# Kernel tuning notes

Hardware: AMD Instinct MI355X
Metric: run time of the kernel (lower is better)

## Reference

```python
import jax, jax.numpy as jnp
import numpy as np

U_NUM, I_NUM, EMBED, NUM_LAYERS = 100000, 50000, 64, 3
N_NODES = U_NUM + I_NUM
BATCH = 8192


def _build_laplacian(rng):
    # Faithful to buildLaplacianMat: symmetric bipartite rating matrix with
    # D^-1/2 A D^-1/2 normalization (degree = count of nonzeros per row).
    nnz = 2_000_000
    u = rng.integers(0, U_NUM, nnz)
    i = rng.integers(0, I_NUM, nnz)
    lin = np.unique(u.astype(np.int64) * I_NUM + i)  # dedupe (user,item) pairs
    u = (lin // I_NUM).astype(np.int32)
    i = (lin % I_NUM).astype(np.int32)
    rating = rng.integers(1, 6, u.shape[0]).astype(np.float32)
    rows = np.concatenate([u, i + U_NUM])
    cols = np.concatenate([i + U_NUM, u])
    vals = np.concatenate([rating, rating])
    deg = np.bincount(rows, minlength=N_NODES)
    dinv = np.where(deg > 0, deg.astype(np.float64) ** -0.5, 0.0).astype(np.float32)
    vals = dinv[rows] * vals * dinv[cols]
    return rows, cols, vals


def setup_inputs() -> dict:
    key = jax.random.key(0)
    k1, k2 = jax.random.split(key)
    rng = np.random.default_rng(0)
    rows, cols, vals = _build_laplacian(rng)
    # xavier_uniform over [num, embed]: bound = sqrt(6/(fan_in+fan_out))
    bu = float(np.sqrt(6.0 / (U_NUM + EMBED)))
    bi = float(np.sqrt(6.0 / (I_NUM + EMBED)))
    uEmbd = jax.random.uniform(k1, (U_NUM, EMBED), jnp.float32, -bu, bu)
    iEmbd = jax.random.uniform(k2, (I_NUM, EMBED), jnp.float32, -bi, bi)
    userIdx = jnp.asarray(rng.integers(0, U_NUM, BATCH), dtype=jnp.int64)
    itemIdx = jnp.asarray(rng.integers(0, I_NUM, BATCH), dtype=jnp.int64)
    return {
        "uEmbd": uEmbd,
        "iEmbd": iEmbd,
        "lap_rows": jnp.asarray(rows, jnp.int32),
        "lap_cols": jnp.asarray(cols, jnp.int32),
        "lap_vals": jnp.asarray(vals, jnp.float32),
        "userIdx": userIdx,
        "itemIdx": itemIdx,
    }


def _spmm(rows, cols, vals, x):
    # sparse [N,N] @ dense [N,D] via edge-list gather + segment-sum
    return jax.ops.segment_sum(vals[:, None] * x[cols], rows, num_segments=N_NODES)


def reference(uEmbd, iEmbd, lap_rows, lap_cols, lap_vals, userIdx, itemIdx):
    feats = jnp.concatenate([uEmbd, iEmbd], axis=0)  # [N, D]
    acc = feats
    f = feats
    for _ in range(NUM_LAYERS):
        f = _spmm(lap_rows, lap_cols, lap_vals, f)
        acc = acc + f
    final = acc / (NUM_LAYERS + 1)  # mean over stacked layer embeddings
    ue = final[userIdx]                      # [B, D]
    ie = final[itemIdx + U_NUM]              # [B, D]
    return jnp.sum(ue * ie, axis=1)          # [B]
```

## Files before the change

kernel.cpp:

```cpp
#include <hip/hip_runtime.h>

#define U_NUMC 100000
#define I_NUMC 50000
#define NNODES 150000
#define EMB 64
#define NBATCH 8192
#define NB_I ((I_NUMC + 255) / 256)

__global__ __launch_bounds__(256) void k_zero(int* __restrict__ p, int n) {
    int i = blockIdx.x * blockDim.x + threadIdx.x;
    if (i < n) p[i] = 0;
}

__global__ __launch_bounds__(256) void k_uptr(const int* __restrict__ rows1, int E1,
                                              int* __restrict__ uptr) {
    int r = blockIdx.x * blockDim.x + threadIdx.x;
    if (r > U_NUMC) return;
    int lo = 0, hi = E1;
    while (lo < hi) {
        int mid = (lo + hi) >> 1;
        if (rows1[mid] < r) lo = mid + 1; else hi = mid;
    }
    uptr[r] = lo;
}

__global__ __launch_bounds__(256) void k_hist(const int* __restrict__ cols1, int E1,
                                              int* __restrict__ hist) {
    int e = blockIdx.x * blockDim.x + threadIdx.x;
    if (e >= E1) return;
    atomicAdd(&hist[cols1[e] - U_NUMC], 1);
}

__global__ __launch_bounds__(256) void k_scan1(const int* __restrict__ hist,
                                               int* __restrict__ bsum) {
    int b = blockIdx.x, t = threadIdx.x;
    int idx = b * 256 + t;
    int v = (idx < I_NUMC) ? hist[idx] : 0;
    #pragma unroll
    for (int o = 32; o; o >>= 1) v += __shfl_xor(v, o);
    __shared__ int ws4[4];
    if ((t & 63) == 0) ws4[t >> 6] = v;
    __syncthreads();
    if (t == 0) bsum[b] = ws4[0] + ws4[1] + ws4[2] + ws4[3];
}

__global__ __launch_bounds__(256) void k_scan2(const int* __restrict__ bsum,
                                               int* __restrict__ boff,
                                               int* __restrict__ iptr) {
    __shared__ int lds[256];
    int t = threadIdx.x;
    int v = (t < NB_I) ? bsum[t] : 0;
    int x = v;
    #pragma unroll
    for (int o = 1; o < 256; o <<= 1) {
        lds[t] = x; __syncthreads();
        int y = (t >= o) ? lds[t - o] : 0; __syncthreads();
        x += y;
    }
    if (t < NB_I) boff[t] = x - v;
    if (t == 255) iptr[I_NUMC] = x;
}

__global__ __launch_bounds__(256) void k_scan3(const int* __restrict__ hist,
                                               const int* __restrict__ boff,
                                               int* __restrict__ iptr,
                                               int* __restrict__ cursor) {
    __shared__ int lds[256];
    int b = blockIdx.x, t = threadIdx.x;
    int idx = b * 256 + t;
    int v = (idx < I_NUMC) ? hist[idx] : 0;
    int x = v;
    #pragma unroll
    for (int o = 1; o < 256; o <<= 1) {
        lds[t] = x; __syncthreads();
        int y = (t >= o) ? lds[t - o] : 0; __syncthreads();
        x += y;
    }
    if (idx < I_NUMC) {
        int excl = boff[b] + x - v;
        iptr[idx] = excl;
        cursor[idx] = excl;
    }
}

__global__ __launch_bounds__(256) void k_scatter(const int* __restrict__ rows1,
                                                 const int* __restrict__ cols1,
                                                 const float* __restrict__ vals1,
                                                 int E1,
                                                 int* __restrict__ cursor,
                                                 int2* __restrict__ item_uv) {
    const int cls  = blockIdx.x & 7;
    const int bsub = blockIdx.x >> 3;
    const int nb   = gridDim.x >> 3;
    const int E4   = E1 >> 2;
    const int4* c4p = (const int4*)cols1;
    for (int q = bsub * 256 + threadIdx.x; q < E4; q += nb * 256) {
        int4 c4 = c4p[q];
        #pragma unroll
        for (int t = 0; t < 4; ++t) {
            int cv = (t == 0) ? c4.x : (t == 1) ? c4.y : (t == 2) ? c4.z : c4.w;
            int i = cv - U_NUMC;
            if (((i >> 3) & 7) != cls) continue;
            int e = q * 4 + t;
            int pos = atomicAdd(&cursor[i], 1);
            item_uv[pos] = make_int2(rows1[e], __float_as_int(vals1[e]));
        }
    }
    if (bsub == 0) {
        int e = E4 * 4 + threadIdx.x;
        if (e < E1) {
            int i = cols1[e] - U_NUMC;
            if (((i >> 3) & 7) == cls) {
                int pos = atomicAdd(&cursor[i], 1);
                item_uv[pos] = make_int2(rows1[e], __float_as_int(vals1[e]));
            }
        }
    }
}

template <int FIRST>
__global__ __launch_bounds__(256) void k_spmm(const float* __restrict__ uE,
                                              const float* __restrict__ iE,
                                              const float* __restrict__ f,
                                              float* __restrict__ fn,
                                              const int* __restrict__ uptr,
                                              const int* __restrict__ cols1,
                                              const float* __restrict__ vals1,
                                              const int* __restrict__ iptr,
                                              const int2* __restrict__ item_uv) {
    int wave = (blockIdx.x * blockDim.x + threadIdx.x) >> 6;
    int lane = threadIdx.x & 63;
    if (wave >= NNODES) return;

    const bool isUser = (wave < U_NUMC);
    int beg, end;
    if (isUser) { beg = uptr[wave];           end = uptr[wave + 1]; }
    else        { int i = wave - U_NUMC; beg = iptr[i]; end = iptr[i + 1]; }
    beg = __builtin_amdgcn_readfirstlane(beg);
    end = __builtin_amdgcn_readfirstlane(end);

    const float* fb;
    if (FIRST) fb = isUser ? (iE - (size_t)U_NUMC * EMB) : uE;
    else       fb = f;

    float s0 = 0.f, s1 = 0.f, s2 = 0.f, s3 = 0.f;
    float s4 = 0.f, s5 = 0.f, s6 = 0.f, s7 = 0.f;
    int j = beg;
    if (isUser) {
        for (; j + 8 <= end; j += 8) {
            #pragma unroll
            for (int t = 0; t < 8; ++t) {
                int   c = cols1[j + t];
                float v = vals1[j + t];
                float l = fb[(size_t)c * EMB + lane];
                if (t == 0) s0 += v * l; else if (t == 1) s1 += v * l;
                else if (t == 2) s2 += v * l; else if (t == 3) s3 += v * l;
                else if (t == 4) s4 += v * l; else if (t == 5) s5 += v * l;
                else if (t == 6) s6 += v * l; else s7 += v * l;
            }
        }
        for (; j < end; ++j)
            s0 += vals1[j] * fb[(size_t)cols1[j] * EMB + lane];
    } else {
        for (; j + 8 <= end; j += 8) {
            #pragma unroll
            for (int t = 0; t < 8; ++t) {
                int2 e = item_uv[j + t];
                float v = __int_as_float(e.y);
                float l = fb[(size_t)e.x * EMB + lane];
                if (t == 0) s0 += v * l; else if (t == 1) s1 += v * l;
                else if (t == 2) s2 += v * l; else if (t == 3) s3 += v * l;
                else if (t == 4) s4 += v * l; else if (t == 5) s5 += v * l;
                else if (t == 6) s6 += v * l; else s7 += v * l;
            }
        }
        for (; j < end; ++j) {
            int2 e = item_uv[j];
            s0 += __int_as_float(e.y) * fb[(size_t)e.x * EMB + lane];
        }
    }
    float sum = ((s0 + s1) + (s2 + s3)) + ((s4 + s5) + (s6 + s7));
    fn[(size_t)wave * EMB + lane] = sum;
}

__global__ __launch_bounds__(256) void k_out(const float* __restrict__ uE,
                                             const float* __restrict__ iE,
                                             const float* __restrict__ g1,
                                             const float* __restrict__ g2,
                                             const float* __restrict__ g3,
                                             const int* __restrict__ userIdx,
                                             const int* __restrict__ itemIdx,
                                             float* __restrict__ out) {
    int wave = (blockIdx.x * blockDim.x + threadIdx.x) >> 6;
    int lane = threadIdx.x & 63;
    if (wave >= NBATCH) return;
    int u  = userIdx[wave];
    int it = itemIdx[wave];
    size_t ou = (size_t)u * EMB + lane;
    size_t oi = (size_t)(U_NUMC + it) * EMB + lane;
    float a = uE[ou] + g1[ou] + g2[ou] + g3[ou];
    float b = iE[(size_t)it * EMB + lane] + g1[oi] + g2[oi] + g3[oi];
    float p = a * b;
    #pragma unroll
    for (int o = 32; o; o >>= 1) p += __shfl_xor(p, o);
    if (lane == 0) out[wave] = p * (1.0f / 16.0f);
}

extern "C" void kernel_launch(void* const* d_in, const int* in_sizes, int n_in,
                              void* d_out, int out_size, void* d_ws, size_t ws_size,
                              hipStream_t stream) {
    const float* uE      = (const float*)d_in[0];
    const float* iE      = (const float*)d_in[1];
    const int*   rows    = (const int*)d_in[2];
    const int*   cols    = (const int*)d_in[3];
    const float* vals    = (const float*)d_in[4];
    const int*   userIdx = (const int*)d_in[5];
    const int*   itemIdx = (const int*)d_in[6];
    const int E  = in_sizes[2];
    const int E1 = E / 2;

    char* ws = (char*)d_ws;
    size_t off = 0;
    auto alloc = [&](size_t bytes) -> void* {
        off = (off + 255) & ~(size_t)255;
        void* p = ws + off;
        off += bytes;
        return p;
    };
    float* g1      = (float*)alloc((size_t)NNODES * EMB * 4);
    float* g2      = (float*)alloc((size_t)NNODES * EMB * 4);
    float* g3      = (float*)alloc((size_t)NNODES * EMB * 4);
    int*   uptr    = (int*)alloc((size_t)(U_NUMC + 1) * 4);
    int*   iptr    = (int*)alloc((size_t)(I_NUMC + 1) * 4);
    int*   hist    = (int*)alloc((size_t)I_NUMC * 4);
    int*   cursor  = (int*)alloc((size_t)I_NUMC * 4);
    int*   bsum    = (int*)alloc((size_t)NB_I * 4);
    int*   boff    = (int*)alloc((size_t)NB_I * 4);
    int2*  item_uv = (int2*)alloc((size_t)E1 * 8);

    k_zero<<<(I_NUMC + 255) / 256, 256, 0, stream>>>(hist, I_NUMC);
    k_uptr<<<(U_NUMC + 256) / 256, 256, 0, stream>>>(rows, E1, uptr);
    k_hist<<<(E1 + 255) / 256, 256, 0, stream>>>(cols, E1, hist);
    k_scan1<<<NB_I, 256, 0, stream>>>(hist, bsum);
    k_scan2<<<1, 256, 0, stream>>>(bsum, boff, iptr);
    k_scan3<<<NB_I, 256, 0, stream>>>(hist, boff, iptr, cursor);
    k_scatter<<<2048, 256, 0, stream>>>(rows, cols, vals, E1, cursor, item_uv);

    const int spmm_blocks = NNODES / 4;
    k_spmm<1><<<spmm_blocks, 256, 0, stream>>>(uE, iE, nullptr, g1,
                                               uptr, cols, vals, iptr, item_uv);
    k_spmm<0><<<spmm_blocks, 256, 0, stream>>>(uE, iE, g1, g2,
                                               uptr, cols, vals, iptr, item_uv);
    k_spmm<0><<<spmm_blocks, 256, 0, stream>>>(uE, iE, g2, g3,
                                               uptr, cols, vals, iptr, item_uv);

    k_out<<<NBATCH / 4, 256, 0, stream>>>(uE, iE, g1, g2, g3,
                                          userIdx, itemIdx, (float*)d_out);
}
```

Measured before the change: 677.4 us.

## Batch 16 gathers per SpMM step, swizzle blocks across XCDs, merge prep kernels

The SpMM inner loop now loads 16 indices and values up front, issues all 16 row gathers, then accumulates, with tail entries masked by clamping the index and zeroing the value. The remainder loop goes away and each wave keeps more loads in flight. Block IDs are remapped so consecutive nodes land on the same XCD, which may improve L2 locality. Fusing the zero and uptr kernels saves one launch, while the larger unrolled arrays add register pressure and wasted gathers for low-degree nodes.

After: 812.3 us. 1.2x slower.

```diff
diff --git a/kernel.cpp b/kernel.cpp
--- a/kernel.cpp
+++ b/kernel.cpp
@@ -6,22 +6,21 @@
 #define EMB 64
 #define NBATCH 8192
 #define NB_I ((I_NUMC + 255) / 256)
-
-__global__ __launch_bounds__(256) void k_zero(int* __restrict__ p, int n) {
-    int i = blockIdx.x * blockDim.x + threadIdx.x;
-    if (i < n) p[i] = 0;
-}
-
-__global__ __launch_bounds__(256) void k_uptr(const int* __restrict__ rows1, int E1,
-                                              int* __restrict__ uptr) {
-    int r = blockIdx.x * blockDim.x + threadIdx.x;
-    if (r > U_NUMC) return;
-    int lo = 0, hi = E1;
-    while (lo < hi) {
-        int mid = (lo + hi) >> 1;
-        if (rows1[mid] < r) lo = mid + 1; else hi = mid;
-    }
-    uptr[r] = lo;
+#define GRP 16
+
+__global__ __launch_bounds__(256) void k_prep(const int* __restrict__ rows1, int E1,
+                                              int* __restrict__ uptr,
+                                              int* __restrict__ hist) {
+    int g = blockIdx.x * blockDim.x + threadIdx.x;
+    if (g < I_NUMC) hist[g] = 0;
+    if (g <= U_NUMC) {
+        int lo = 0, hi = E1;
+        while (lo < hi) {
+            int mid = (lo + hi) >> 1;
+            if (rows1[mid] < g) lo = mid + 1; else hi = mid;
+        }
+        uptr[g] = lo;
+    }
 }
 
 __global__ __launch_bounds__(256) void k_hist(const int* __restrict__ cols1, int E1,
@@ -128,7 +127,12 @@
                                               const float* __restrict__ vals1,
                                               const int* __restrict__ iptr,
                                               const int2* __restrict__ item_uv) {
-    int wave = (blockIdx.x * blockDim.x + threadIdx.x) >> 6;
+    int nwg = gridDim.x;
+    int q = nwg >> 3, r = nwg & 7;
+    int xcd = blockIdx.x & 7, sub = blockIdx.x >> 3;
+    int swz = (xcd < r ? xcd * (q + 1) : r * (q + 1) + (xcd - r) * q) + sub;
+
+    int wave = ((swz << 8) + (int)threadIdx.x) >> 6;
     int lane = threadIdx.x & 63;
     if (wave >= NNODES) return;
 
@@ -143,43 +147,51 @@
     if (FIRST) fb = isUser ? (iE - (size_t)U_NUMC * EMB) : uE;
     else       fb = f;
 
-    float s0 = 0.f, s1 = 0.f, s2 = 0.f, s3 = 0.f;
-    float s4 = 0.f, s5 = 0.f, s6 = 0.f, s7 = 0.f;
-    int j = beg;
+    float s[GRP];
+    #pragma unroll
+    for (int t = 0; t < GRP; ++t) s[t] = 0.f;
+
     if (isUser) {
-        for (; j + 8 <= end; j += 8) {
-            #pragma unroll
-            for (int t = 0; t < 8; ++t) {
-                int   c = cols1[j + t];
-                float v = vals1[j + t];
-                float l = fb[(size_t)c * EMB + lane];
-                if (t == 0) s0 += v * l; else if (t == 1) s1 += v * l;
-                else if (t == 2) s2 += v * l; else if (t == 3) s3 += v * l;
-                else if (t == 4) s4 += v * l; else if (t == 5) s5 += v * l;
-                else if (t == 6) s6 += v * l; else s7 += v * l;
+        for (int j = beg; j < end; j += GRP) {
+            int   cc[GRP];
+            float vv[GRP];
+            #pragma unroll
+            for (int t = 0; t < GRP; ++t) {
+                int idx = j + t;
+                int ld = min(idx, end - 1);
+                cc[t] = cols1[ld];
+                vv[t] = (idx < end) ? vals1[ld] : 0.f;
             }
-        }
-        for (; j < end; ++j)
-            s0 += vals1[j] * fb[(size_t)cols1[j] * EMB + lane];
+            float l[GRP];
+            #pragma unroll
+            for (int t = 0; t < GRP; ++t)
+                l[t] = fb[(size_t)cc[t] * EMB + lane];
+            #pragma unroll
+            for (int t = 0; t < GRP; ++t) s[t] += vv[t] * l[t];
+        }
     } else {
-        for (; j + 8 <= end; j += 8) {
-            #pragma unroll
-            for (int t = 0; t < 8; ++t) {
-                int2 e = item_uv[j + t];
-                float v = __int_as_float(e.y);
-                float l = fb[(size_t)e.x * EMB + lane];
-                if (t == 0) s0 += v * l; else if (t == 1) s1 += v * l;
-                else if (t == 2) s2 += v * l; else if (t == 3) s3 += v * l;
-                else if (t == 4) s4 += v * l; else if (t == 5) s5 += v * l;
-                else if (t == 6) s6 += v * l; else s7 += v * l;
+        for (int j = beg; j < end; j += GRP) {
+            int   cc[GRP];
+            float vv[GRP];
+            #pragma unroll
+            for (int t = 0; t < GRP; ++t) {
+                int idx = j + t;
+                int ld = min(idx, end - 1);
+                int2 e = item_uv[ld];
+                cc[t] = e.x;
+                vv[t] = (idx < end) ? __int_as_float(e.y) : 0.f;
             }
-        }
-        for (; j < end; ++j) {
-            int2 e = item_uv[j];
-            s0 += __int_as_float(e.y) * fb[(size_t)e.x * EMB + lane];
-        }
-    }
-    float sum = ((s0 + s1) + (s2 + s3)) + ((s4 + s5) + (s6 + s7));
+            float l[GRP];
+            #pragma unroll
+            for (int t = 0; t < GRP; ++t)
+                l[t] = fb[(size_t)cc[t] * EMB + lane];
+            #pragma unroll
+            for (int t = 0; t < GRP; ++t) s[t] += vv[t] * l[t];
+        }
+    }
+    float sum = 0.f;
+    #pragma unroll
+    for (int t = 0; t < GRP; ++t) sum += s[t];
     fn[(size_t)wave * EMB + lane] = sum;
 }
 
@@ -238,8 +250,7 @@
     int*   boff    = (int*)alloc((size_t)NB_I * 4);
     int2*  item_uv = (int2*)alloc((size_t)E1 * 8);
 
-    k_zero<<<(I_NUMC + 255) / 256, 256, 0, stream>>>(hist, I_NUMC);
-    k_uptr<<<(U_NUMC + 256) / 256, 256, 0, stream>>>(rows, E1, uptr);
+    k_prep<<<(U_NUMC + 256) / 256, 256, 0, stream>>>(rows, E1, uptr, hist);
     k_hist<<<(E1 + 255) / 256, 256, 0, stream>>>(cols, E1, hist);
     k_scan1<<<NB_I, 256, 0, stream>>>(hist, bsum);
     k_scan2<<<1, 256, 0, stream>>>(bsum, boff, iptr);
```

## Overlap item CSR scatter with user-side first SpMM layer; merge zero and uptr kernels

Applied to the files above, without the earlier changes.

The user rows of the first propagation layer only need the row-sorted COO and uptr, not the transposed item list. They are now computed inside the same launch as the item scatter, using extra blocks, so that gather work overlaps the atomic scatter. The item rows of layer one run in a separate kernel afterwards. The histogram zeroing is also folded into the uptr binary-search kernel to drop a launch. The cost is a more heterogeneous fused kernel whose two block types compete for bandwidth and scheduling.

Measured after the change: 671.2 us. No clear change (-0.9%).

```diff
diff --git a/kernel.cpp b/kernel.cpp
--- a/kernel.cpp
+++ b/kernel.cpp
@@ -6,22 +6,21 @@
 #define EMB 64
 #define NBATCH 8192
 #define NB_I ((I_NUMC + 255) / 256)
-
-__global__ __launch_bounds__(256) void k_zero(int* __restrict__ p, int n) {
-    int i = blockIdx.x * blockDim.x + threadIdx.x;
-    if (i < n) p[i] = 0;
-}
-
-__global__ __launch_bounds__(256) void k_uptr(const int* __restrict__ rows1, int E1,
-                                              int* __restrict__ uptr) {
-    int r = blockIdx.x * blockDim.x + threadIdx.x;
-    if (r > U_NUMC) return;
-    int lo = 0, hi = E1;
-    while (lo < hi) {
-        int mid = (lo + hi) >> 1;
-        if (rows1[mid] < r) lo = mid + 1; else hi = mid;
-    }
-    uptr[r] = lo;
+#define SCAT_NB 2048
+
+__global__ __launch_bounds__(256) void k_prep(const int* __restrict__ rows1, int E1,
+                                              int* __restrict__ uptr,
+                                              int* __restrict__ hist) {
+    int g = blockIdx.x * blockDim.x + threadIdx.x;
+    if (g < I_NUMC) hist[g] = 0;
+    if (g <= U_NUMC) {
+        int lo = 0, hi = E1;
+        while (lo < hi) {
+            int mid = (lo + hi) >> 1;
+            if (rows1[mid] < g) lo = mid + 1; else hi = mid;
+        }
+        uptr[g] = lo;
+    }
 }
 
 __global__ __launch_bounds__(256) void k_hist(const int* __restrict__ cols1, int E1,
@@ -83,70 +82,55 @@
     }
 }
 
-__global__ __launch_bounds__(256) void k_scatter(const int* __restrict__ rows1,
-                                                 const int* __restrict__ cols1,
-                                                 const float* __restrict__ vals1,
-                                                 int E1,
-                                                 int* __restrict__ cursor,
-                                                 int2* __restrict__ item_uv) {
-    const int cls  = blockIdx.x & 7;
-    const int bsub = blockIdx.x >> 3;
-    const int nb   = gridDim.x >> 3;
-    const int E4   = E1 >> 2;
-    const int4* c4p = (const int4*)cols1;
-    for (int q = bsub * 256 + threadIdx.x; q < E4; q += nb * 256) {
-        int4 c4 = c4p[q];
-        #pragma unroll
-        for (int t = 0; t < 4; ++t) {
-            int cv = (t == 0) ? c4.x : (t == 1) ? c4.y : (t == 2) ? c4.z : c4.w;
-            int i = cv - U_NUMC;
-            if (((i >> 3) & 7) != cls) continue;
-            int e = q * 4 + t;
-            int pos = atomicAdd(&cursor[i], 1);
-            item_uv[pos] = make_int2(rows1[e], __float_as_int(vals1[e]));
-        }
-    }
-    if (bsub == 0) {
-        int e = E4 * 4 + threadIdx.x;
-        if (e < E1) {
-            int i = cols1[e] - U_NUMC;
-            if (((i >> 3) & 7) == cls) {
+__global__ __launch_bounds__(256) void k_scat_userL1(const int* __restrict__ rows1,
+                                                     const int* __restrict__ cols1,
+                                                     const float* __restrict__ vals1,
+                                                     int E1,
+                                                     int* __restrict__ cursor,
+                                                     int2* __restrict__ item_uv,
+                                                     const float* __restrict__ uE,
+                                                     const float* __restrict__ iE,
+                                                     float* __restrict__ g1,
+                                                     const int* __restrict__ uptr) {
+    if (blockIdx.x < SCAT_NB) {
+        const int cls  = blockIdx.x & 7;
+        const int bsub = blockIdx.x >> 3;
+        const int nb   = SCAT_NB >> 3;
+        const int E4   = E1 >> 2;
+        const int4* c4p = (const int4*)cols1;
+        for (int q = bsub * 256 + (int)threadIdx.x; q < E4; q += nb * 256) {
+            int4 c4 = c4p[q];
+            #pragma unroll
+            for (int t = 0; t < 4; ++t) {
+                int cv = (t == 0) ? c4.x : (t == 1) ? c4.y : (t == 2) ? c4.z : c4.w;
+                int i = cv - U_NUMC;
+                if (((i >> 3) & 7) != cls) continue;
+                int e = q * 4 + t;
                 int pos = atomicAdd(&cursor[i], 1);
                 item_uv[pos] = make_int2(rows1[e], __float_as_int(vals1[e]));
             }
         }
-    }
-}
-
-template <int FIRST>
-__global__ __launch_bounds__(256) void k_spmm(const float* __restrict__ uE,
-                                              const float* __restrict__ iE,
-                                              const float* __restrict__ f,
-                                              float* __restrict__ fn,
-                                              const int* __restrict__ uptr,
-                                              const int* __restrict__ cols1,
-                                              const float* __restrict__ vals1,
-                                              const int* __restrict__ iptr,
-                                              const int2* __restrict__ item_uv) {
-    int wave = (blockIdx.x * blockDim.x + threadIdx.x) >> 6;
-    int lane = threadIdx.x & 63;
-    if (wave >= NNODES) return;
-
-    const bool isUser = (wave < U_NUMC);
-    int beg, end;
-    if (isUser) { beg = uptr[wave];           end = uptr[wave + 1]; }
-    else        { int i = wave - U_NUMC; beg = iptr[i]; end = iptr[i + 1]; }
-    beg = __builtin_amdgcn_readfirstlane(beg);
-    end = __builtin_amdgcn_readfirstlane(end);
-
-    const float* fb;
-    if (FIRST) fb = isUser ? (iE - (size_t)U_NUMC * EMB) : uE;
-    else       fb = f;
-
-    float s0 = 0.f, s1 = 0.f, s2 = 0.f, s3 = 0.f;
-    float s4 = 0.f, s5 = 0.f, s6 = 0.f, s7 = 0.f;
-    int j = beg;
-    if (isUser) {
+        if (bsub == 0) {
+            int e = E4 * 4 + (int)threadIdx.x;
+            if (e < E1) {
+                int i = cols1[e] - U_NUMC;
+                if (((i >> 3) & 7) == cls) {
+                    int pos = atomicAdd(&cursor[i], 1);
+                    item_uv[pos] = make_int2(rows1[e], __float_as_int(vals1[e]));
+                }
+            }
+        }
+    } else {
+        int w = ((blockIdx.x - SCAT_NB) * 256 + (int)threadIdx.x) >> 6;
+        if (w >= U_NUMC) return;
+        int lane = threadIdx.x & 63;
+        int beg = uptr[w], end = uptr[w + 1];
+        beg = __builtin_amdgcn_readfirstlane(beg);
+        end = __builtin_amdgcn_readfirstlane(end);
+        const float* fb = iE - (size_t)U_NUMC * EMB;
+        float s0 = 0.f, s1 = 0.f, s2 = 0.f, s3 = 0.f;
+        float s4 = 0.f, s5 = 0.f, s6 = 0.f, s7 = 0.f;
+        int j = beg;
         for (; j + 8 <= end; j += 8) {
             #pragma unroll
             for (int t = 0; t < 8; ++t) {
@@ -161,13 +145,87 @@
         }
         for (; j < end; ++j)
             s0 += vals1[j] * fb[(size_t)cols1[j] * EMB + lane];
+        float sum = ((s0 + s1) + (s2 + s3)) + ((s4 + s5) + (s6 + s7));
+        g1[(size_t)w * EMB + lane] = sum;
+    }
+}
+
+__global__ __launch_bounds__(256) void k_spmm_itemL1(const float* __restrict__ uE,
+                                                     float* __restrict__ g1,
+                                                     const int* __restrict__ iptr,
+                                                     const int2* __restrict__ item_uv) {
+    int w = (blockIdx.x * 256 + (int)threadIdx.x) >> 6;
+    if (w >= I_NUMC) return;
+    int lane = threadIdx.x & 63;
+    int beg = iptr[w], end = iptr[w + 1];
+    beg = __builtin_amdgcn_readfirstlane(beg);
+    end = __builtin_amdgcn_readfirstlane(end);
+    float s0 = 0.f, s1 = 0.f, s2 = 0.f, s3 = 0.f;
+    float s4 = 0.f, s5 = 0.f, s6 = 0.f, s7 = 0.f;
+    int j = beg;
+    for (; j + 8 <= end; j += 8) {
+        #pragma unroll
+        for (int t = 0; t < 8; ++t) {
+            int2 e = item_uv[j + t];
+            float v = __int_as_float(e.y);
+            float l = uE[(size_t)e.x * EMB + lane];
+            if (t == 0) s0 += v * l; else if (t == 1) s1 += v * l;
+            else if (t == 2) s2 += v * l; else if (t == 3) s3 += v * l;
+            else if (t == 4) s4 += v * l; else if (t == 5) s5 += v * l;
+            else if (t == 6) s6 += v * l; else s7 += v * l;
+        }
+    }
+    for (; j < end; ++j) {
+        int2 e = item_uv[j];
+        s0 += __int_as_float(e.y) * uE[(size_t)e.x * EMB + lane];
+    }
+    float sum = ((s0 + s1) + (s2 + s3)) + ((s4 + s5) + (s6 + s7));
+    g1[(size_t)(U_NUMC + w) * EMB + lane] = sum;
+}
+
+__global__ __launch_bounds__(256) void k_spmm(const float* __restrict__ f,
+                                              float* __restrict__ fn,
+                                              const int* __restrict__ uptr,
+                                              const int* __restrict__ cols1,
+                                              const float* __restrict__ vals1,
+                                              const int* __restrict__ iptr,
+                                              const int2* __restrict__ item_uv) {
+    int wave = (blockIdx.x * blockDim.x + threadIdx.x) >> 6;
+    int lane = threadIdx.x & 63;
+    if (wave >= NNODES) return;
+
+    const bool isUser = (wave < U_NUMC);
+    int beg, end;
+    if (isUser) { beg = uptr[wave];           end = uptr[wave + 1]; }
+    else        { int i = wave - U_NUMC; beg = iptr[i]; end = iptr[i + 1]; }
+    beg = __builtin_amdgcn_readfirstlane(beg);
+    end = __builtin_amdgcn_readfirstlane(end);
+
+    float s0 = 0.f, s1 = 0.f, s2 = 0.f, s3 = 0.f;
+    float s4 = 0.f, s5 = 0.f, s6 = 0.f, s7 = 0.f;
+    int j = beg;
+    if (isUser) {
+        for (; j + 8 <= end; j += 8) {
+            #pragma unroll
+            for (int t = 0; t < 8; ++t) {
+                int   c = cols1[j + t];
+                float v = vals1[j + t];
+                float l = f[(size_t)c * EMB + lane];
+                if (t == 0) s0 += v * l; else if (t == 1) s1 += v * l;
+                else if (t == 2) s2 += v * l; else if (t == 3) s3 += v * l;
+                else if (t == 4) s4 += v * l; else if (t == 5) s5 += v * l;
+                else if (t == 6) s6 += v * l; else s7 += v * l;
+            }
+        }
+        for (; j < end; ++j)
+            s0 += vals1[j] * f[(size_t)cols1[j] * EMB + lane];
     } else {
         for (; j + 8 <= end; j += 8) {
             #pragma unroll
             for (int t = 0; t < 8; ++t) {
                 int2 e = item_uv[j + t];
                 float v = __int_as_float(e.y);
-                float l = fb[(size_t)e.x * EMB + lane];
+                float l = f[(size_t)e.x * EMB + lane];
                 if (t == 0) s0 += v * l; else if (t == 1) s1 += v * l;
                 else if (t == 2) s2 += v * l; else if (t == 3) s3 += v * l;
                 else if (t == 4) s4 += v * l; else if (t == 5) s5 += v * l;
@@ -176,7 +234,7 @@
         }
         for (; j < end; ++j) {
             int2 e = item_uv[j];
-            s0 += __int_as_float(e.y) * fb[(size_t)e.x * EMB + lane];
+            s0 += __int_as_float(e.y) * f[(size_t)e.x * EMB + lane];
         }
     }
     float sum = ((s0 + s1) + (s2 + s3)) + ((s4 + s5) + (s6 + s7));
@@ -238,21 +296,19 @@
     int*   boff    = (int*)alloc((size_t)NB_I * 4);
     int2*  item_uv = (int2*)alloc((size_t)E1 * 8);
 
-    k_zero<<<(I_NUMC + 255) / 256, 256, 0, stream>>>(hist, I_NUMC);
-    k_uptr<<<(U_NUMC + 256) / 256, 256, 0, stream>>>(rows, E1, uptr);
+    k_prep<<<(U_NUMC + 256) / 256, 256, 0, stream>>>(rows, E1, uptr, hist);
     k_hist<<<(E1 + 255) / 256, 256, 0, stream>>>(cols, E1, hist);
     k_scan1<<<NB_I, 256, 0, stream>>>(hist, bsum);
     k_scan2<<<1, 256, 0, stream>>>(bsum, boff, iptr);
     k_scan3<<<NB_I, 256, 0, stream>>>(hist, boff, iptr, cursor);
-    k_scatter<<<2048, 256, 0, stream>>>(rows, cols, vals, E1, cursor, item_uv);
-
-    const int spmm_blocks = NNODES / 4;
-    k_spmm<1><<<spmm_blocks, 256, 0, stream>>>(uE, iE, nullptr, g1,
-                                               uptr, cols, vals, iptr, item_uv);
-    k_spmm<0><<<spmm_blocks, 256, 0, stream>>>(uE, iE, g1, g2,
-                                               uptr, cols, vals, iptr, item_uv);
-    k_spmm<0><<<spmm_blocks, 256, 0, stream>>>(uE, iE, g2, g3,
-                                               uptr, cols, vals, iptr, item_uv);
+
+    const int userL1_blocks = U_NUMC / 4;
+    k_scat_userL1<<<SCAT_NB + userL1_blocks, 256, 0, stream>>>(
+        rows, cols, vals, E1, cursor, item_uv, uE, iE, g1, uptr);
+
+    k_spmm_itemL1<<<I_NUMC / 4, 256, 0, stream>>>(uE, g1, iptr, item_uv);
+    k_spmm<<<NNODES / 4, 256, 0, stream>>>(g1, g2, uptr, cols, vals, iptr, item_uv);
+    k_spmm<<<NNODES / 4, 256, 0, stream>>>(g2, g3, uptr, cols, vals, iptr, item_uv);
 
     k_out<<<NBATCH / 4, 256, 0, stream>>>(uE, iE, g1, g2, g3,
                                           userIdx, itemIdx, (float*)d_out);
```
